# Kernel tuning notes

Measured on AMD Instinct MI355X. Metric: run time of the kernel, lower is better.

The kernel has to match this reference:

```python
import jax, jax.numpy as jnp
import numpy as np

N, D, L, H = 4, 512, 2048, 8  # batch, feat_dim, seq_len, num_heads


def setup_inputs() -> dict:
    key = jax.random.key(0)
    k1, k2, k3, k4 = jax.random.split(key, 4)
    x = jax.random.normal(k1, (N, D, L), dtype=jnp.float32)
    w_qkv = jax.random.normal(k2, (3 * D, D, 1), dtype=jnp.float32) * 0.02   # 1x1 conv
    w_dw = jax.random.normal(k3, (3 * D, 1, 3), dtype=jnp.float32) * 0.02    # depthwise k=3
    w_proj = jax.random.normal(k4, (D, D, 1), dtype=jnp.float32) * 0.02      # 1x1 conv
    temperature = jnp.ones((1, H, 1, 1), dtype=jnp.float32)
    return {"x": x, "w_qkv": w_qkv, "w_dw": w_dw, "w_proj": w_proj, "temperature": temperature}


def _conv1x1(x, w):
    # x: (n, c_in, l), w: (c_out, c_in, 1)
    return jnp.einsum('oc,ncl->nol', w[:, :, 0], x)


def _l2norm(t, eps=1e-12):
    # matches F.normalize: t / max(||t||_2, eps) along last dim
    n = jnp.sqrt(jnp.sum(t * t, axis=-1, keepdims=True))
    return t / jnp.maximum(n, eps)


def reference(x, w_qkv, w_dw, w_proj, temperature):
    n, d, l = x.shape
    h = temperature.shape[1]
    dh = d // h

    qkv = _conv1x1(x, w_qkv)                               # (n, 3d, l)
    qkv = jax.lax.conv_general_dilated(
        qkv, w_dw, window_strides=(1,), padding=[(1, 1)],
        dimension_numbers=('NCH', 'OIH', 'NCH'),
        feature_group_count=3 * d)                          # depthwise conv, (n, 3d, l)

    q, k, v = jnp.split(qkv, 3, axis=1)                     # each (n, d, l)
    # (n, d, l) -> (n, h, dh, l) -> (n, h, l, dh)
    q = q.reshape(n, h, dh, l).transpose(0, 1, 3, 2)
    k = k.reshape(n, h, dh, l).transpose(0, 1, 3, 2)
    v = v.reshape(n, h, dh, l).transpose(0, 1, 3, 2)

    q = _l2norm(q)
    k = _l2norm(k)

    scores = jnp.einsum('nhqd,nhkd->nhqk', q, k) * temperature  # (n, h, l, l)
    attn = jax.nn.softmax(scores, axis=-1)
    out = jnp.einsum('nhqk,nhkd->nhqd', attn, v)                # (n, h, l, dh)
    out = out.transpose(0, 1, 3, 2).reshape(n, d, l)            # (n, d, l)
    return _conv1x1(out, w_proj)
```

## Files before the change

### kernel.cpp

```cpp
#include <hip/hip_runtime.h>
#include <hip/hip_bf16.h>
#include <cstdint>
#include <cstddef>

#define N_B 4
#define D_F 512
#define L_S 2048
#define H_N 8
#define DH  64
#define C3  (3*D_F)

typedef __attribute__((ext_vector_type(8)))  short short8;
typedef __attribute__((ext_vector_type(4)))  float f32x4;
typedef __attribute__((ext_vector_type(16))) float f32x16;

__device__ __forceinline__ unsigned int pk_bf16(float a, float b) {
    __hip_bfloat162 h = __float22bfloat162_rn(float2{a, b});
    union { __hip_bfloat162 h; unsigned int u; } cv;
    cv.h = h;
    return cv.u;
}
__device__ __forceinline__ unsigned short bf16_rn(float f) {
    union { float f; unsigned int u; } c; c.f = f;
    unsigned int r = c.u + 0x7FFF + ((c.u >> 16) & 1);
    return (unsigned short)(r >> 16);
}
__device__ __forceinline__ float bf16_f(unsigned short h) {
    union { unsigned int u; float f; } c; c.u = ((unsigned int)h) << 16;
    return c.f;
}

__device__ __forceinline__ void gll16(const unsigned short* g, unsigned short* l) {
    __builtin_amdgcn_global_load_lds(
        (const __attribute__((address_space(1))) unsigned int*)g,
        (__attribute__((address_space(3))) unsigned int*)l,
        16, 0, 0);
}

__global__ __launch_bounds__(256) void cvt_split(const float* __restrict__ src,
                                                 unsigned short* __restrict__ hi,
                                                 unsigned short* __restrict__ lo,
                                                 int n4) {
    int i = blockIdx.x * 256 + threadIdx.x;
    if (i >= n4) return;
    float4 v = ((const float4*)src)[i];
    ushort4 h, l;
    h.x = bf16_rn(v.x); l.x = bf16_rn(v.x - bf16_f(h.x));
    h.y = bf16_rn(v.y); l.y = bf16_rn(v.y - bf16_f(h.y));
    h.z = bf16_rn(v.z); l.z = bf16_rn(v.z - bf16_f(h.z));
    h.w = bf16_rn(v.w); l.w = bf16_rn(v.w - bf16_f(h.w));
    ((ushort4*)hi)[i] = h;
    ((ushort4*)lo)[i] = l;
}

__global__ __launch_bounds__(256) void cvt_xT(const float* __restrict__ x,
                                              unsigned short* __restrict__ xT,
                                              int C) {
    __shared__ float tile[64][65];
    const int tid = threadIdx.x;
    const int l0  = blockIdx.x * 64;
    const int c0  = blockIdx.y * 64;
    const int n   = blockIdx.z;

    const float* xn = x + (size_t)n * C * L_S;
#pragma unroll
    for (int r = 0; r < 16; ++r) {
        int c = r * 4 + (tid >> 6);
        int l = tid & 63;
        tile[c][l] = xn[(size_t)(c0 + c) * L_S + l0 + l];
    }
    __syncthreads();

    unsigned short* xn_t = xT + (size_t)n * L_S * C;
#pragma unroll
    for (int r = 0; r < 8; ++r) {
        int l  = r * 8 + (tid >> 5);
        int cp = tid & 31;
        unsigned int pk = pk_bf16(tile[cp * 2][l], tile[cp * 2 + 1][l]);
        *(unsigned int*)&xn_t[(size_t)(l0 + l) * C + c0 + cp * 2] = pk;
    }
}

template<int SPLIT, int OUT_BF16>
__global__ __launch_bounds__(256) void gemm_mfma2(const unsigned short* __restrict__ Whi,
                                                  const unsigned short* __restrict__ Wlo,
                                                  const unsigned short* __restrict__ XThi,
                                                  const unsigned short* __restrict__ XTlo,
                                                  void* __restrict__ Y,
                                                  int O, int C) {
    __shared__ unsigned short Wt[SPLIT ? 2 : 1][4][128 * 8];
    __shared__ unsigned short Xt[SPLIT ? 2 : 1][4][128 * 8];

    const int tid  = threadIdx.x;
    const int lane = tid & 63;
    const int w    = tid >> 6;
    const int g    = lane >> 4;
    const int c    = lane & 15;
    const int wr   = (w >> 1) * 64;
    const int wc   = (w & 1) * 64;
    const int l0   = blockIdx.x * 128;
    const int o0   = blockIdx.y * 128;
    const int n    = blockIdx.z;

    const unsigned short* XTn_hi = XThi + (size_t)n * L_S * C;
    const unsigned short* XTn_lo = SPLIT ? (XTlo + (size_t)n * L_S * C) : nullptr;

    const int rhalf = (w & 1) * 64;
    const int cpA   = w >> 1;
    const int cpB   = 2 + (w >> 1);
    const size_t wrowA = (size_t)(o0 + rhalf + lane) * C;
    const size_t xrowA = (size_t)(l0 + rhalf + lane) * C;

    f32x4 acc[4][4];
#pragma unroll
    for (int mt = 0; mt < 4; ++mt)
#pragma unroll
        for (int nt = 0; nt < 4; ++nt) acc[mt][nt] = (f32x4){0.f, 0.f, 0.f, 0.f};

    for (int c0 = 0; c0 < C; c0 += 32) {
        __syncthreads();
        gll16(Whi + wrowA + c0 + cpA * 8, &Wt[0][cpA][rhalf * 8]);
        gll16(Whi + wrowA + c0 + cpB * 8, &Wt[0][cpB][rhalf * 8]);
        gll16(XTn_hi + xrowA + c0 + cpA * 8, &Xt[0][cpA][rhalf * 8]);
        gll16(XTn_hi + xrowA + c0 + cpB * 8, &Xt[0][cpB][rhalf * 8]);
        if (SPLIT) {
            gll16(Wlo + wrowA + c0 + cpA * 8, &Wt[1][cpA][rhalf * 8]);
            gll16(Wlo + wrowA + c0 + cpB * 8, &Wt[1][cpB][rhalf * 8]);
            gll16(XTn_lo + xrowA + c0 + cpA * 8, &Xt[1][cpA][rhalf * 8]);
            gll16(XTn_lo + xrowA + c0 + cpB * 8, &Xt[1][cpB][rhalf * 8]);
        }
        __syncthreads();

        short8 a0[4], b0[4];
#pragma unroll
        for (int mt = 0; mt < 4; ++mt) a0[mt] = *(short8*)&Wt[0][g][(wr + mt * 16 + c) * 8];
#pragma unroll
        for (int nt = 0; nt < 4; ++nt) b0[nt] = *(short8*)&Xt[0][g][(wc + nt * 16 + c) * 8];

        if (SPLIT) {
            short8 a1[4], b1[4];
#pragma unroll
            for (int mt = 0; mt < 4; ++mt) a1[mt] = *(short8*)&Wt[1][g][(wr + mt * 16 + c) * 8];
#pragma unroll
            for (int nt = 0; nt < 4; ++nt) b1[nt] = *(short8*)&Xt[1][g][(wc + nt * 16 + c) * 8];
#pragma unroll
            for (int mt = 0; mt < 4; ++mt)
#pragma unroll
                for (int nt = 0; nt < 4; ++nt) {
                    acc[mt][nt] = __builtin_amdgcn_mfma_f32_16x16x32_bf16(a0[mt], b0[nt], acc[mt][nt], 0, 0, 0);
                    acc[mt][nt] = __builtin_amdgcn_mfma_f32_16x16x32_bf16(a0[mt], b1[nt], acc[mt][nt], 0, 0, 0);
                    acc[mt][nt] = __builtin_amdgcn_mfma_f32_16x16x32_bf16(a1[mt], b0[nt], acc[mt][nt], 0, 0, 0);
                }
        } else {
#pragma unroll
            for (int mt = 0; mt < 4; ++mt)
#pragma unroll
                for (int nt = 0; nt < 4; ++nt)
                    acc[mt][nt] = __builtin_amdgcn_mfma_f32_16x16x32_bf16(a0[mt], b0[nt], acc[mt][nt], 0, 0, 0);
        }
    }

#pragma unroll
    for (int mt = 0; mt < 4; ++mt) {
#pragma unroll
        for (int r = 0; r < 4; ++r) {
            int oo = o0 + wr + mt * 16 + g * 4 + r;
            size_t rowbase = ((size_t)n * O + oo) * L_S;
#pragma unroll
            for (int nt = 0; nt < 4; ++nt) {
                int ll = l0 + wc + nt * 16 + c;
                if (OUT_BF16)
                    ((unsigned short*)Y)[rowbase + ll] = bf16_rn(acc[mt][nt][r]);
                else
                    ((float*)Y)[rowbase + ll] = acc[mt][nt][r];
            }
        }
    }
}

__global__ __launch_bounds__(256) void fused_qk2(const unsigned short* __restrict__ qkv_bf,
                                                 const float* __restrict__ w_dw,
                                                 unsigned short* __restrict__ Qb,
                                                 unsigned short* __restrict__ Kb) {
    __shared__ unsigned short rows[64 * 264];
    __shared__ float wsm[192];
    const int tid = threadIdx.x;
    const int l0  = blockIdx.x * 256;
    const int gg  = blockIdx.y;
    const int n   = blockIdx.z;
    const int head = gg & 7;
    const int ch0  = (gg < 8) ? head * 64 : 512 + head * 64;

    if (tid < 192) wsm[tid] = w_dw[ch0 * 3 + tid];

    const unsigned short* base = qkv_bf + ((size_t)n * C3 + ch0) * L_S;
    for (int f = tid; f < 2048; f += 256) {
        int e = f >> 5, s = f & 31;
        *(uint4*)&rows[e * 264 + s * 8] = *(const uint4*)&base[(size_t)e * L_S + l0 + s * 8];
    }
    if (tid < 64) {
        rows[tid * 264 + 256] = (l0 > 0) ? base[(size_t)tid * L_S + l0 - 1] : (unsigned short)0;
    } else if (tid < 128) {
        int e = tid - 64;
        rows[e * 264 + 257] = (l0 + 256 < L_S) ? base[(size_t)e * L_S + l0 + 256] : (unsigned short)0;
    }
    __syncthreads();

    const int lL = tid;
    const int iL = (lL == 0)   ? 256 : lL - 1;
    const int iR = (lL == 255) ? 257 : lL + 1;
    float y[64];
    float s = 0.f;
#pragma unroll
    for (int e = 0; e < 64; ++e) {
        float a = bf16_f(rows[e * 264 + iL]);
        float b = bf16_f(rows[e * 264 + lL]);
        float d = bf16_f(rows[e * 264 + iR]);
        float v = wsm[e * 3 + 0] * a + wsm[e * 3 + 1] * b + wsm[e * 3 + 2] * d;
        y[e] = v;
        s += v * v;
    }
    float sc = 1.0f / fmaxf(sqrtf(s), 1e-12f);

    const int l = l0 + tid;
    unsigned short* dst = ((gg < 8) ? Qb : Kb) + (size_t)(n * H_N + head) * 8 * L_S * 8;
#pragma unroll
    for (int p = 0; p < 8; ++p) {
        uint4 pk = make_uint4(pk_bf16(y[8 * p + 0] * sc, y[8 * p + 1] * sc),
                              pk_bf16(y[8 * p + 2] * sc, y[8 * p + 3] * sc),
                              pk_bf16(y[8 * p + 4] * sc, y[8 * p + 5] * sc),
                              pk_bf16(y[8 * p + 6] * sc, y[8 * p + 7] * sc));
        *(uint4*)&dst[((size_t)p * L_S + l) * 8] = pk;
    }
}

__global__ __launch_bounds__(256) void fused_v2(const unsigned short* __restrict__ qkv_bf,
                                                const float* __restrict__ w_dw,
                                                unsigned short* __restrict__ Vb) {
    const int tid = threadIdx.x;
    const int e   = tid & 63;
    const int jp  = blockIdx.x * 4 + (tid >> 6);
    const int h   = blockIdx.y;
    const int n   = blockIdx.z;
    const int ch  = 1024 + h * 64 + e;
    const unsigned short* row = qkv_bf + ((size_t)n * C3 + ch) * L_S;
    const int k0 = jp * 8;

    uint4 mv = *(const uint4*)&row[k0];
    unsigned int lw = (jp > 0)   ? *(const unsigned int*)&row[k0 - 2] : 0u;
    unsigned int rw = (jp < 255) ? *(const unsigned int*)&row[k0 + 8] : 0u;

    float v[10];
    v[0] = bf16_f((unsigned short)(lw >> 16));
    v[1] = bf16_f((unsigned short)(mv.x & 0xFFFF));
    v[2] = bf16_f((unsigned short)(mv.x >> 16));
    v[3] = bf16_f((unsigned short)(mv.y & 0xFFFF));
    v[4] = bf16_f((unsigned short)(mv.y >> 16));
    v[5] = bf16_f((unsigned short)(mv.z & 0xFFFF));
    v[6] = bf16_f((unsigned short)(mv.z >> 16));
    v[7] = bf16_f((unsigned short)(mv.w & 0xFFFF));
    v[8] = bf16_f((unsigned short)(mv.w >> 16));
    v[9] = bf16_f((unsigned short)(rw & 0xFFFF));

    float w0 = w_dw[ch * 3 + 0], w1 = w_dw[ch * 3 + 1], w2 = w_dw[ch * 3 + 2];
    unsigned int o[4];
#pragma unroll
    for (int i = 0; i < 4; ++i) {
        float y0 = w0 * v[2 * i + 0] + w1 * v[2 * i + 1] + w2 * v[2 * i + 2];
        float y1 = w0 * v[2 * i + 1] + w1 * v[2 * i + 2] + w2 * v[2 * i + 3];
        o[i] = pk_bf16(y0, y1);
    }
    uint4 ov = make_uint4(o[0], o[1], o[2], o[3]);
    *(uint4*)&Vb[(((size_t)(n * H_N + h) * 256 + jp) * 512) + e * 8] = ov;
}

__global__ __launch_bounds__(256) void attn6(const unsigned short* __restrict__ Qb,
                                             const unsigned short* __restrict__ Kb,
                                             const unsigned short* __restrict__ Vb,
                                             const float* __restrict__ temp,
                                             unsigned short* __restrict__ aoT_hi,
                                             unsigned short* __restrict__ aoT_lo) {
    __shared__ unsigned short KV[32768];
    __shared__ float sm[128];
    float* Ot = (float*)KV;

    const int tid  = threadIdx.x;
    const int lane = tid & 63;
    const int w    = tid >> 6;
    const int c32  = lane & 31;
    const int h    = lane >> 5;
    const int q0   = blockIdx.x * 128;
    const int hd   = blockIdx.y;
    const int n    = blockIdx.z;

    const size_t hb = (size_t)(n * H_N + hd);
    const unsigned short* Qh = Qb + hb * 8 * L_S * 8;
    const unsigned short* Kh = Kb + hb * 8 * L_S * 8;
    const unsigned short* Vh = Vb + hb * 256 * 512;
    const float t    = temp[hd];
    const float negm = -fabsf(t);

    unsigned short* Qs = KV + 16384;
    {
        int idx = w * 4;
#pragma unroll
        for (int r = 0; r < 4; ++r) {
            int p = (idx + r) >> 1, hh = (idx + r) & 1;
            gll16(Qh + ((size_t)p * L_S + q0 + hh * 64 + lane) * 8, Qs + p * 1024 + hh * 512);
        }
        gll16(Kh + ((size_t)w * L_S + lane) * 8,              KV + w * 512);
        gll16(Kh + ((size_t)(w + 4) * L_S + lane) * 8,        KV + (w + 4) * 512);
        gll16(Vh + ((size_t)w * 512 + lane * 8),              KV + 4096 + w * 512);
        gll16(Vh + ((size_t)(w + 4) * 512 + lane * 8),        KV + 4096 + (w + 4) * 512);
        gll16(Kh + ((size_t)w * L_S + 64 + lane) * 8,         KV + 8192 + w * 512);
        gll16(Kh + ((size_t)(w + 4) * L_S + 64 + lane) * 8,   KV + 8192 + (w + 4) * 512);
        gll16(Vh + ((size_t)(8 + w) * 512 + lane * 8),        KV + 12288 + w * 512);
        gll16(Vh + ((size_t)(8 + w + 4) * 512 + lane * 8),    KV + 12288 + (w + 4) * 512);
    }
    __syncthreads();
    short8 qa[4];
#pragma unroll
    for (int es = 0; es < 4; ++es)
        qa[es] = *(short8*)&Qs[(es * 2 + h) * 1024 + (w * 32 + c32) * 8];
    __syncthreads();

    f32x16 acc0, acc1;
#pragma unroll
    for (int i = 0; i < 16; ++i) { acc0[i] = 0.f; acc1[i] = 0.f; }
    float sumP = 0.f;

#define SM_BLOCK(SF0, SF1, PA)                                                  \
    {                                                                           \
        unsigned int W_[16], R_[16];                                            \
        _Pragma("unroll")                                                       \
        for (int G = 0; G < 4; ++G) {                                           \
            float p0 = __expf(fmaf((SF0)[4*G+0], t, negm));                     \
            float p1 = __expf(fmaf((SF0)[4*G+1], t, negm));                     \
            float p2 = __expf(fmaf((SF0)[4*G+2], t, negm));                     \
            float p3 = __expf(fmaf((SF0)[4*G+3], t, negm));                     \
            sumP += (p0 + p1) + (p2 + p3);                                      \
            W_[2*G]   = pk_bf16(p0, p1);                                        \
            W_[2*G+1] = pk_bf16(p2, p3);                                        \
            float u0 = __expf(fmaf((SF1)[4*G+0], t, negm));                     \
            float u1 = __expf(fmaf((SF1)[4*G+1], t, negm));                     \
            float u2 = __expf(fmaf((SF1)[4*G+2], t, negm));                     \
            float u3 = __expf(fmaf((SF1)[4*G+3], t, negm));                     \
            sumP += (u0 + u1) + (u2 + u3);                                      \
            W_[8+2*G]   = pk_bf16(u0, u1);                                      \
            W_[8+2*G+1] = pk_bf16(u2, u3);                                      \
        }                                                                       \
        _Pragma("unroll")                                                       \
        for (int j = 0; j < 16; ++j) R_[j] = __shfl_xor(W_[j], 32);             \
        _Pragma("unroll")                                                       \
        for (int ks = 0; ks < 4; ++ks) {                                        \
            const int bb = (ks >> 1) * 8;                                       \
            const int m4 = (ks & 1) * 4;                                        \
            unsigned int a0 = h ? R_[bb+m4+2] : W_[bb+m4+0];                    \
            unsigned int a1 = h ? R_[bb+m4+3] : W_[bb+m4+1];                    \
            unsigned int a2 = h ? W_[bb+m4+2] : R_[bb+m4+0];                    \
            unsigned int a3 = h ? W_[bb+m4+3] : R_[bb+m4+1];                    \
            uint4 pu = make_uint4(a0, a1, a2, a3);                              \
            (PA)[ks] = *(short8*)&pu;                                           \
        }                                                                       \
    }

    for (int it = 0; it < 16; ++it) {
        const int cur = it & 1;
        const unsigned short* B = KV + cur * 16384;

        if (it < 15) {
            const int kb = (it + 1) * 128;
            unsigned short* D = KV + (cur ^ 1) * 16384;
            gll16(Kh + ((size_t)w * L_S + kb + lane) * 8,                D + w * 512);
            gll16(Kh + ((size_t)(w + 4) * L_S + kb + lane) * 8,          D + (w + 4) * 512);
            gll16(Vh + ((size_t)(kb / 8 + w) * 512 + lane * 8),          D + 4096 + w * 512);
            gll16(Vh + ((size_t)(kb / 8 + w + 4) * 512 + lane * 8),      D + 4096 + (w + 4) * 512);
            gll16(Kh + ((size_t)w * L_S + kb + 64 + lane) * 8,           D + 8192 + w * 512);
            gll16(Kh + ((size_t)(w + 4) * L_S + kb + 64 + lane) * 8,     D + 8192 + (w + 4) * 512);
            gll16(Vh + ((size_t)(kb / 8 + 8 + w) * 512 + lane * 8),      D + 12288 + w * 512);
            gll16(Vh + ((size_t)(kb / 8 + 8 + w + 4) * 512 + lane * 8),  D + 12288 + (w + 4) * 512);
        }

        f32x16 sa0, sa1, sb0, sb1;
#pragma unroll
        for (int i = 0; i < 16; ++i) { sa0[i] = 0.f; sa1[i] = 0.f; sb0[i] = 0.f; sb1[i] = 0.f; }
#pragma unroll
        for (int es = 0; es < 4; ++es) {
            short8 k0f = *(short8*)&B[(es * 2 + h) * 512 + c32 * 8];
            short8 k1f = *(short8*)&B[(es * 2 + h) * 512 + (32 + c32) * 8];
            sa0 = __builtin_amdgcn_mfma_f32_32x32x16_bf16(k0f, qa[es], sa0, 0, 0, 0);
            sa1 = __builtin_amdgcn_mfma_f32_32x32x16_bf16(k1f, qa[es], sa1, 0, 0, 0);
        }
#pragma unroll
        for (int es = 0; es < 4; ++es) {
            short8 k0f = *(short8*)&B[8192 + (es * 2 + h) * 512 + c32 * 8];
            short8 k1f = *(short8*)&B[8192 + (es * 2 + h) * 512 + (32 + c32) * 8];
            sb0 = __builtin_amdgcn_mfma_f32_32x32x16_bf16(k0f, qa[es], sb0, 0, 0, 0);
            sb1 = __builtin_amdgcn_mfma_f32_32x32x16_bf16(k1f, qa[es], sb1, 0, 0, 0);
        }

        short8 paA[4];
        SM_BLOCK(sa0, sa1, paA)

#pragma unroll
        for (int ks = 0; ks < 4; ++ks) {
            short8 vb0 = *(short8*)&B[4096 + (ks * 2 + h) * 512 + c32 * 8];
            short8 vb1 = *(short8*)&B[4096 + (ks * 2 + h) * 512 + (32 + c32) * 8];
            acc0 = __builtin_amdgcn_mfma_f32_32x32x16_bf16(paA[ks], vb0, acc0, 0, 0, 0);
            acc1 = __builtin_amdgcn_mfma_f32_32x32x16_bf16(paA[ks], vb1, acc1, 0, 0, 0);
        }

        short8 paB[4];
        SM_BLOCK(sb0, sb1, paB)

#pragma unroll
        for (int ks = 0; ks < 4; ++ks) {
            short8 vb0 = *(short8*)&B[12288 + (ks * 2 + h) * 512 + c32 * 8];
            short8 vb1 = *(short8*)&B[12288 + (ks * 2 + h) * 512 + (32 + c32) * 8];
            acc0 = __builtin_amdgcn_mfma_f32_32x32x16_bf16(paB[ks], vb0, acc0, 0, 0, 0);
            acc1 = __builtin_amdgcn_mfma_f32_32x32x16_bf16(paB[ks], vb1, acc1, 0, 0, 0);
        }

        __syncthreads();
    }
#undef SM_BLOCK

    sumP += __shfl_xor(sumP, 32);
    sm[w * 32 + c32] = 1.0f / sumP;

    float inv[16];
#pragma unroll
    for (int r = 0; r < 16; ++r) {
        int ql = (r & 3) + 8 * (r >> 2) + 4 * h;
        inv[r] = sm[w * 32 + ql];
    }

#pragma unroll
    for (int r = 0; r < 16; ++r) {
        int ql = (r & 3) + 8 * (r >> 2) + 4 * h;
        int qg = w * 32 + ql;
        Ot[qg * 64 + (c32 ^ (qg & 31))]        = acc0[r] * inv[r];
        Ot[qg * 64 + ((32 + c32) ^ (qg & 31))] = acc1[r] * inv[r];
    }
    __syncthreads();

    for (int tt = tid; tt < 8192; tt += 256) {
        int qq = tt >> 6, e = tt & 63;
        float v = Ot[qq * 64 + (e ^ (qq & 31))];
        unsigned short hi_ = bf16_rn(v);
        unsigned short lo_ = bf16_rn(v - bf16_f(hi_));
        size_t off = ((size_t)n * L_S + q0 + qq) * D_F + hd * 64 + e;
        aoT_hi[off] = hi_;
        aoT_lo[off] = lo_;
    }
}

extern "C" void kernel_launch(void* const* d_in, const int* in_sizes, int n_in,
                              void* d_out, int out_size, void* d_ws, size_t ws_size,
                              hipStream_t stream) {
    const float* x      = (const float*)d_in[0];
    const float* w_qkv  = (const float*)d_in[1];
    const float* w_dw   = (const float*)d_in[2];
    const float* w_proj = (const float*)d_in[3];
    const float* temp   = (const float*)d_in[4];
    float* out = (float*)d_out;

    const size_t WQE = (size_t)C3 * D_F;
    const size_t WPE = (size_t)D_F * D_F;

    char* ws = (char*)d_ws;
    unsigned short* qkv_bf = (unsigned short*)ws;
    unsigned short* Qb     = (unsigned short*)(ws + 25165824);
    unsigned short* Kb     = (unsigned short*)(ws + 33554432);
    unsigned short* Vb     = (unsigned short*)(ws + 41943040);
    unsigned short* xT     = (unsigned short*)(ws + 50331648);
    unsigned short* aoT_lo = (unsigned short*)(ws + 58720256);
    unsigned short* wq_hi  = (unsigned short*)(ws + 67108864);
    unsigned short* wq_lo  = wq_hi + WQE;
    unsigned short* wp_hi  = (unsigned short*)(ws + 70254592);
    unsigned short* wp_lo  = wp_hi + WPE;
    unsigned short* aoT_hi = xT;

    cvt_xT<<<dim3(L_S / 64, D_F / 64, N_B), 256, 0, stream>>>(x, xT, D_F);
    cvt_split<<<dim3((WQE / 4 + 255) / 256), 256, 0, stream>>>(w_qkv, wq_hi, wq_lo, WQE / 4);
    cvt_split<<<dim3((WPE / 4 + 255) / 256), 256, 0, stream>>>(w_proj, wp_hi, wp_lo, WPE / 4);

    gemm_mfma2<0, 1><<<dim3(L_S / 128, C3 / 128, N_B), 256, 0, stream>>>(
        wq_hi, nullptr, xT, nullptr, qkv_bf, C3, D_F);

    fused_qk2<<<dim3(L_S / 256, 16, N_B), 256, 0, stream>>>(qkv_bf, w_dw, Qb, Kb);
    fused_v2<<<dim3(64, H_N, N_B), 256, 0, stream>>>(qkv_bf, w_dw, Vb);

    attn6<<<dim3(L_S / 128, H_N, N_B), 256, 0, stream>>>(Qb, Kb, Vb, temp, aoT_hi, aoT_lo);

    gemm_mfma2<1, 0><<<dim3(L_S / 128, D_F / 128, N_B), 256, 0, stream>>>(
        wp_hi, wp_lo, aoT_hi, aoT_lo, out, D_F, D_F);
}
```

Before: 159.8 us.

## Split attention KV loop across two wave groups with 512-thread blocks

The attention kernel now runs 8 waves per block instead of 4. The waves form two groups that each handle alternating 64-key chunks of the sequence with their own double-buffered K/V tiles, and the groups combine partial output accumulators and softmax sums through shared memory at the end. This raises the number of waves per CU available to hide latency and shortens each wave's serial loop. In exchange it adds a cross-group reduction, an extra barrier and more LDS traffic, and launch bounds may limit registers per thread.

```diff
diff --git a/kernel.cpp b/kernel.cpp
--- a/kernel.cpp
+++ b/kernel.cpp
@@ -274,19 +274,22 @@
     *(uint4*)&Vb[(((size_t)(n * H_N + h) * 256 + jp) * 512) + e * 8] = ov;
 }
 
-__global__ __launch_bounds__(256) void attn6(const unsigned short* __restrict__ Qb,
-                                             const unsigned short* __restrict__ Kb,
-                                             const unsigned short* __restrict__ Vb,
-                                             const float* __restrict__ temp,
-                                             unsigned short* __restrict__ aoT_hi,
-                                             unsigned short* __restrict__ aoT_lo) {
+__global__ __launch_bounds__(512, 4) void attn7(const unsigned short* __restrict__ Qb,
+                                                const unsigned short* __restrict__ Kb,
+                                                const unsigned short* __restrict__ Vb,
+                                                const float* __restrict__ temp,
+                                                unsigned short* __restrict__ aoT_hi,
+                                                unsigned short* __restrict__ aoT_lo) {
     __shared__ unsigned short KV[32768];
-    __shared__ float sm[128];
-    float* Ot = (float*)KV;
+    __shared__ float smA[128], smB[128];
+    float* OtB = (float*)(KV + 16384);
+    float* OtA = (float*)KV;
 
     const int tid  = threadIdx.x;
     const int lane = tid & 63;
     const int w    = tid >> 6;
+    const int g2   = w >> 2;
+    const int wv   = w & 3;
     const int c32  = lane & 31;
     const int h    = lane >> 5;
     const int q0   = blockIdx.x * 128;
@@ -300,28 +303,33 @@
     const float t    = temp[hd];
     const float negm = -fabsf(t);
 
-    unsigned short* Qs = KV + 16384;
-    {
-        int idx = w * 4;
-#pragma unroll
-        for (int r = 0; r < 4; ++r) {
-            int p = (idx + r) >> 1, hh = (idx + r) & 1;
+    unsigned short* myKV = KV + g2 * 16384;
+    unsigned short* Qs   = KV + 24576;
+
+    for (int tk = w; tk < 48; tk += 8) {
+        if (tk < 16) {
+            int p = tk >> 1, hh = tk & 1;
             gll16(Qh + ((size_t)p * L_S + q0 + hh * 64 + lane) * 8, Qs + p * 1024 + hh * 512);
-        }
-        gll16(Kh + ((size_t)w * L_S + lane) * 8,              KV + w * 512);
-        gll16(Kh + ((size_t)(w + 4) * L_S + lane) * 8,        KV + (w + 4) * 512);
-        gll16(Vh + ((size_t)w * 512 + lane * 8),              KV + 4096 + w * 512);
-        gll16(Vh + ((size_t)(w + 4) * 512 + lane * 8),        KV + 4096 + (w + 4) * 512);
-        gll16(Kh + ((size_t)w * L_S + 64 + lane) * 8,         KV + 8192 + w * 512);
-        gll16(Kh + ((size_t)(w + 4) * L_S + 64 + lane) * 8,   KV + 8192 + (w + 4) * 512);
-        gll16(Vh + ((size_t)(8 + w) * 512 + lane * 8),        KV + 12288 + w * 512);
-        gll16(Vh + ((size_t)(8 + w + 4) * 512 + lane * 8),    KV + 12288 + (w + 4) * 512);
-    }
-    __syncthreads();
+        } else if (tk < 24) {
+            int p = tk - 16;
+            gll16(Kh + ((size_t)p * L_S + lane) * 8, KV + p * 512);
+        } else if (tk < 32) {
+            int p = tk - 24;
+            gll16(Vh + ((size_t)p * 512 + lane * 8), KV + 4096 + p * 512);
+        } else if (tk < 40) {
+            int p = tk - 32;
+            gll16(Kh + ((size_t)p * L_S + 64 + lane) * 8, KV + 16384 + p * 512);
+        } else {
+            int p = tk - 40;
+            gll16(Vh + ((size_t)(8 + p) * 512 + lane * 8), KV + 16384 + 4096 + p * 512);
+        }
+    }
+    __syncthreads();
+
     short8 qa[4];
 #pragma unroll
     for (int es = 0; es < 4; ++es)
-        qa[es] = *(short8*)&Qs[(es * 2 + h) * 1024 + (w * 32 + c32) * 8];
+        qa[es] = *(short8*)&Qs[(es * 2 + h) * 1024 + (wv * 32 + c32) * 8];
     __syncthreads();
 
     f32x16 acc0, acc1;
@@ -329,124 +337,109 @@
     for (int i = 0; i < 16; ++i) { acc0[i] = 0.f; acc1[i] = 0.f; }
     float sumP = 0.f;
 
-#define SM_BLOCK(SF0, SF1, PA)                                                  \
-    {                                                                           \
-        unsigned int W_[16], R_[16];                                            \
-        _Pragma("unroll")                                                       \
-        for (int G = 0; G < 4; ++G) {                                           \
-            float p0 = __expf(fmaf((SF0)[4*G+0], t, negm));                     \
-            float p1 = __expf(fmaf((SF0)[4*G+1], t, negm));                     \
-            float p2 = __expf(fmaf((SF0)[4*G+2], t, negm));                     \
-            float p3 = __expf(fmaf((SF0)[4*G+3], t, negm));                     \
-            sumP += (p0 + p1) + (p2 + p3);                                      \
-            W_[2*G]   = pk_bf16(p0, p1);                                        \
-            W_[2*G+1] = pk_bf16(p2, p3);                                        \
-            float u0 = __expf(fmaf((SF1)[4*G+0], t, negm));                     \
-            float u1 = __expf(fmaf((SF1)[4*G+1], t, negm));                     \
-            float u2 = __expf(fmaf((SF1)[4*G+2], t, negm));                     \
-            float u3 = __expf(fmaf((SF1)[4*G+3], t, negm));                     \
-            sumP += (u0 + u1) + (u2 + u3);                                      \
-            W_[8+2*G]   = pk_bf16(u0, u1);                                      \
-            W_[8+2*G+1] = pk_bf16(u2, u3);                                      \
-        }                                                                       \
-        _Pragma("unroll")                                                       \
-        for (int j = 0; j < 16; ++j) R_[j] = __shfl_xor(W_[j], 32);             \
-        _Pragma("unroll")                                                       \
-        for (int ks = 0; ks < 4; ++ks) {                                        \
-            const int bb = (ks >> 1) * 8;                                       \
-            const int m4 = (ks & 1) * 4;                                        \
-            unsigned int a0 = h ? R_[bb+m4+2] : W_[bb+m4+0];                    \
-            unsigned int a1 = h ? R_[bb+m4+3] : W_[bb+m4+1];                    \
-            unsigned int a2 = h ? W_[bb+m4+2] : R_[bb+m4+0];                    \
-            unsigned int a3 = h ? W_[bb+m4+3] : R_[bb+m4+1];                    \
-            uint4 pu = make_uint4(a0, a1, a2, a3);                              \
-            (PA)[ks] = *(short8*)&pu;                                           \
-        }                                                                       \
-    }
-
     for (int it = 0; it < 16; ++it) {
         const int cur = it & 1;
-        const unsigned short* B = KV + cur * 16384;
+        const unsigned short* B = myKV + cur * 8192;
 
         if (it < 15) {
-            const int kb = (it + 1) * 128;
-            unsigned short* D = KV + (cur ^ 1) * 16384;
-            gll16(Kh + ((size_t)w * L_S + kb + lane) * 8,                D + w * 512);
-            gll16(Kh + ((size_t)(w + 4) * L_S + kb + lane) * 8,          D + (w + 4) * 512);
-            gll16(Vh + ((size_t)(kb / 8 + w) * 512 + lane * 8),          D + 4096 + w * 512);
-            gll16(Vh + ((size_t)(kb / 8 + w + 4) * 512 + lane * 8),      D + 4096 + (w + 4) * 512);
-            gll16(Kh + ((size_t)w * L_S + kb + 64 + lane) * 8,           D + 8192 + w * 512);
-            gll16(Kh + ((size_t)(w + 4) * L_S + kb + 64 + lane) * 8,     D + 8192 + (w + 4) * 512);
-            gll16(Vh + ((size_t)(kb / 8 + 8 + w) * 512 + lane * 8),      D + 12288 + w * 512);
-            gll16(Vh + ((size_t)(kb / 8 + 8 + w + 4) * 512 + lane * 8),  D + 12288 + (w + 4) * 512);
-        }
-
-        f32x16 sa0, sa1, sb0, sb1;
-#pragma unroll
-        for (int i = 0; i < 16; ++i) { sa0[i] = 0.f; sa1[i] = 0.f; sb0[i] = 0.f; sb1[i] = 0.f; }
+            const int kb = ((it + 1) * 2 + g2) * 64;
+            unsigned short* D = myKV + (cur ^ 1) * 8192;
+            gll16(Kh + ((size_t)wv * L_S + kb + lane) * 8,            D + wv * 512);
+            gll16(Kh + ((size_t)(wv + 4) * L_S + kb + lane) * 8,      D + (wv + 4) * 512);
+            gll16(Vh + ((size_t)(kb / 8 + wv) * 512 + lane * 8),      D + 4096 + wv * 512);
+            gll16(Vh + ((size_t)(kb / 8 + wv + 4) * 512 + lane * 8),  D + 4096 + (wv + 4) * 512);
+        }
+
+        f32x16 sf0, sf1;
+#pragma unroll
+        for (int i = 0; i < 16; ++i) { sf0[i] = 0.f; sf1[i] = 0.f; }
 #pragma unroll
         for (int es = 0; es < 4; ++es) {
-            short8 k0f = *(short8*)&B[(es * 2 + h) * 512 + c32 * 8];
-            short8 k1f = *(short8*)&B[(es * 2 + h) * 512 + (32 + c32) * 8];
-            sa0 = __builtin_amdgcn_mfma_f32_32x32x16_bf16(k0f, qa[es], sa0, 0, 0, 0);
-            sa1 = __builtin_amdgcn_mfma_f32_32x32x16_bf16(k1f, qa[es], sa1, 0, 0, 0);
-        }
-#pragma unroll
-        for (int es = 0; es < 4; ++es) {
-            short8 k0f = *(short8*)&B[8192 + (es * 2 + h) * 512 + c32 * 8];
-            short8 k1f = *(short8*)&B[8192 + (es * 2 + h) * 512 + (32 + c32) * 8];
-            sb0 = __builtin_amdgcn_mfma_f32_32x32x16_bf16(k0f, qa[es], sb0, 0, 0, 0);
-            sb1 = __builtin_amdgcn_mfma_f32_32x32x16_bf16(k1f, qa[es], sb1, 0, 0, 0);
-        }
-
-        short8 paA[4];
-        SM_BLOCK(sa0, sa1, paA)
+            short8 ka0 = *(short8*)&B[(es * 2 + h) * 512 + c32 * 8];
+            short8 ka1 = *(short8*)&B[(es * 2 + h) * 512 + (32 + c32) * 8];
+            sf0 = __builtin_amdgcn_mfma_f32_32x32x16_bf16(ka0, qa[es], sf0, 0, 0, 0);
+            sf1 = __builtin_amdgcn_mfma_f32_32x32x16_bf16(ka1, qa[es], sf1, 0, 0, 0);
+        }
+
+        short8 pa[4];
+        {
+            unsigned int W_[16], R_[16];
+#pragma unroll
+            for (int G = 0; G < 4; ++G) {
+                float p0 = __expf(fmaf(sf0[4*G+0], t, negm));
+                float p1 = __expf(fmaf(sf0[4*G+1], t, negm));
+                float p2 = __expf(fmaf(sf0[4*G+2], t, negm));
+                float p3 = __expf(fmaf(sf0[4*G+3], t, negm));
+                sumP += (p0 + p1) + (p2 + p3);
+                W_[2*G]   = pk_bf16(p0, p1);
+                W_[2*G+1] = pk_bf16(p2, p3);
+                float u0 = __expf(fmaf(sf1[4*G+0], t, negm));
+                float u1 = __expf(fmaf(sf1[4*G+1], t, negm));
+                float u2 = __expf(fmaf(sf1[4*G+2], t, negm));
+                float u3 = __expf(fmaf(sf1[4*G+3], t, negm));
+                sumP += (u0 + u1) + (u2 + u3);
+                W_[8+2*G]   = pk_bf16(u0, u1);
+                W_[8+2*G+1] = pk_bf16(u2, u3);
+            }
+#pragma unroll
+            for (int j = 0; j < 16; ++j) R_[j] = __shfl_xor(W_[j], 32);
+#pragma unroll
+            for (int ks = 0; ks < 4; ++ks) {
+                const int bb = (ks >> 1) * 8;
+                const int m4 = (ks & 1) * 4;
+                unsigned int a0 = h ? R_[bb+m4+2] : W_[bb+m4+0];
+                unsigned int a1 = h ? R_[bb+m4+3] : W_[bb+m4+1];
+                unsigned int a2 = h ? W_[bb+m4+2] : R_[bb+m4+0];
+                unsigned int a3 = h ? W_[bb+m4+3] : R_[bb+m4+1];
+                uint4 pu = make_uint4(a0, a1, a2, a3);
+                pa[ks] = *(short8*)&pu;
+            }
+        }
 
 #pragma unroll
         for (int ks = 0; ks < 4; ++ks) {
             short8 vb0 = *(short8*)&B[4096 + (ks * 2 + h) * 512 + c32 * 8];
             short8 vb1 = *(short8*)&B[4096 + (ks * 2 + h) * 512 + (32 + c32) * 8];
-            acc0 = __builtin_amdgcn_mfma_f32_32x32x16_bf16(paA[ks], vb0, acc0, 0, 0, 0);
-            acc1 = __builtin_amdgcn_mfma_f32_32x32x16_bf16(paA[ks], vb1, acc1, 0, 0, 0);
-        }
-
-        short8 paB[4];
-        SM_BLOCK(sb0, sb1, paB)
-
-#pragma unroll
-        for (int ks = 0; ks < 4; ++ks) {
-            short8 vb0 = *(short8*)&B[12288 + (ks * 2 + h) * 512 + c32 * 8];
-            short8 vb1 = *(short8*)&B[12288 + (ks * 2 + h) * 512 + (32 + c32) * 8];
-            acc0 = __builtin_amdgcn_mfma_f32_32x32x16_bf16(paB[ks], vb0, acc0, 0, 0, 0);
-            acc1 = __builtin_amdgcn_mfma_f32_32x32x16_bf16(paB[ks], vb1, acc1, 0, 0, 0);
+            acc0 = __builtin_amdgcn_mfma_f32_32x32x16_bf16(pa[ks], vb0, acc0, 0, 0, 0);
+            acc1 = __builtin_amdgcn_mfma_f32_32x32x16_bf16(pa[ks], vb1, acc1, 0, 0, 0);
         }
 
         __syncthreads();
     }
-#undef SM_BLOCK
 
     sumP += __shfl_xor(sumP, 32);
-    sm[w * 32 + c32] = 1.0f / sumP;
-
-    float inv[16];
-#pragma unroll
-    for (int r = 0; r < 16; ++r) {
-        int ql = (r & 3) + 8 * (r >> 2) + 4 * h;
-        inv[r] = sm[w * 32 + ql];
-    }
-
-#pragma unroll
-    for (int r = 0; r < 16; ++r) {
-        int ql = (r & 3) + 8 * (r >> 2) + 4 * h;
-        int qg = w * 32 + ql;
-        Ot[qg * 64 + (c32 ^ (qg & 31))]        = acc0[r] * inv[r];
-        Ot[qg * 64 + ((32 + c32) ^ (qg & 31))] = acc1[r] * inv[r];
-    }
-    __syncthreads();
-
-    for (int tt = tid; tt < 8192; tt += 256) {
+
+    if (g2 == 1) {
+        smB[wv * 32 + c32] = sumP;
+#pragma unroll
+        for (int r = 0; r < 16; ++r) {
+            int ql = (r & 3) + 8 * (r >> 2) + 4 * h;
+            int qg = wv * 32 + ql;
+            OtB[qg * 64 + c32]      = acc0[r];
+            OtB[qg * 64 + 32 + c32] = acc1[r];
+        }
+    } else {
+        smA[wv * 32 + c32] = sumP;
+    }
+    __syncthreads();
+
+    if (g2 == 0) {
+#pragma unroll
+        for (int r = 0; r < 16; ++r) {
+            int ql = (r & 3) + 8 * (r >> 2) + 4 * h;
+            int qg = wv * 32 + ql;
+            float inv = 1.0f / (smA[qg] + smB[qg]);
+            float v0 = (acc0[r] + OtB[qg * 64 + c32])      * inv;
+            float v1 = (acc1[r] + OtB[qg * 64 + 32 + c32]) * inv;
+            OtA[qg * 64 + (c32 ^ (qg & 31))]        = v0;
+            OtA[qg * 64 + ((32 + c32) ^ (qg & 31))] = v1;
+        }
+    }
+    __syncthreads();
+
+    for (int tt = tid; tt < 8192; tt += 512) {
         int qq = tt >> 6, e = tt & 63;
-        float v = Ot[qq * 64 + (e ^ (qq & 31))];
+        float v = OtA[qq * 64 + (e ^ (qq & 31))];
         unsigned short hi_ = bf16_rn(v);
         unsigned short lo_ = bf16_rn(v - bf16_f(hi_));
         size_t off = ((size_t)n * L_S + q0 + qq) * D_F + hd * 64 + e;
@@ -491,7 +484,7 @@
     fused_qk2<<<dim3(L_S / 256, 16, N_B), 256, 0, stream>>>(qkv_bf, w_dw, Qb, Kb);
     fused_v2<<<dim3(64, H_N, N_B), 256, 0, stream>>>(qkv_bf, w_dw, Vb);
 
-    attn6<<<dim3(L_S / 128, H_N, N_B), 256, 0, stream>>>(Qb, Kb, Vb, temp, aoT_hi, aoT_lo);
+    attn7<<<dim3(L_S / 128, H_N, N_B), 512, 0, stream>>>(Qb, Kb, Vb, temp, aoT_hi, aoT_lo);
 
     gemm_mfma2<1, 0><<<dim3(L_S / 128, D_F / 128, N_B), 256, 0, stream>>>(
         wp_hi, wp_lo, aoT_hi, aoT_lo, out, D_F, D_F);
```

New measurement: 152.2 us. 4.7% less time.
